# Performance work log

Hardware: AMD Instinct MI355X
Metric: run time of the kernel (lower is better)

The kernel has to match this reference:

```python
import jax, jax.numpy as jnp
import numpy as np

N = 50000
E = 600000


def gcn_conv(x, W, b, src, dst, n):
    # PyG GCNConv: h = x @ W; add self-loops; symmetric normalization; aggregate; + bias
    h = x @ W  # [N, out]
    deg = jnp.zeros((n,), h.dtype).at[dst].add(1.0) + 1.0  # self-loop included
    dinv = jax.lax.rsqrt(deg)  # deg >= 1, always finite
    coef = dinv[src] * dinv[dst]  # [E]
    msg = h[src] * coef[:, None]  # [E, out]  (the memory-bound gather)
    agg = jax.ops.segment_sum(msg, dst, num_segments=n)
    agg = agg + h * (dinv * dinv)[:, None]  # self-loop contribution
    return agg + b


def setup_inputs() -> dict:
    key = jax.random.key(0)
    ks = jax.random.split(key, 8)
    x = jax.random.normal(ks[0], (N, 128), dtype=jnp.float32)
    edge_index = jax.random.randint(ks[1], (2, E), 0, N, dtype=jnp.int64 if jax.config.jax_enable_x64 else jnp.int32)
    def glorot(k, fan_in, fan_out):
        s = jnp.sqrt(6.0 / (fan_in + fan_out))
        return jax.random.uniform(k, (fan_in, fan_out), jnp.float32, -s, s)
    W1 = glorot(ks[2], 128, 128)
    b1 = jnp.zeros((128,), jnp.float32)
    W2 = glorot(ks[3], 128, 64)
    b2 = jnp.zeros((64,), jnp.float32)
    W3 = glorot(ks[4], 64, 16)
    b3 = jnp.zeros((16,), jnp.float32)
    return {"x": x, "edge_index": edge_index, "W1": W1, "b1": b1, "W2": W2, "b2": b2, "W3": W3, "b3": b3}


def reference(x, edge_index, W1, b1, W2, b2, W3, b3):
    src, dst = edge_index[0], edge_index[1]
    n = x.shape[0]
    h = jax.nn.relu(gcn_conv(x, W1, b1, src, dst, n))
    h = jax.nn.relu(gcn_conv(h, W2, b2, src, dst, n))
    h = gcn_conv(h, W3, b3, src, dst, n)
    return h
```

## Files before the change

kernel.cpp:

```cpp
#include <hip/hip_runtime.h>
#include <hip/hip_fp16.h>
#include <type_traits>


typedef _Float16 f16x8 __attribute__((ext_vector_type(8)));
typedef float f32x4 __attribute__((ext_vector_type(4)));

#define CSR_CAP 32

__device__ inline float2 h2f(unsigned int u) {
  __half2 h = __builtin_bit_cast(__half2, u);
  return __half22float2(h);
}

__device__ inline void fma8h(float4& a0, float4& a1, const uint4& g, float w) {
  float2 f0 = h2f(g.x), f1 = h2f(g.y), f2 = h2f(g.z), f3 = h2f(g.w);
  a0.x = fmaf(f0.x, w, a0.x);
  a0.y = fmaf(f0.y, w, a0.y);
  a0.z = fmaf(f1.x, w, a0.z);
  a0.w = fmaf(f1.y, w, a0.w);
  a1.x = fmaf(f2.x, w, a1.x);
  a1.y = fmaf(f2.y, w, a1.y);
  a1.z = fmaf(f3.x, w, a1.z);
  a1.w = fmaf(f3.y, w, a1.w);
}

__device__ inline unsigned int pack2h(float x, float y) {
  __half2 h = __floats2half2_rn(x, y);
  return __builtin_bit_cast(unsigned int, h);
}

__device__ inline uint2 pack4h(const float4& v) {
  uint2 r;
  r.x = pack2h(v.x, v.y);
  r.y = pack2h(v.z, v.w);
  return r;
}

template <int K, int F, typename TIN>
__global__ __launch_bounds__(512) void gemm_mfma(const TIN* __restrict__ A,
                                                 const float* __restrict__ W,
                                                 __half* __restrict__ C16, int n,
                                                 int nwaves,
                                                 const int* __restrict__ src,
                                                 const int* __restrict__ dst,
                                                 int* __restrict__ cur,
                                                 unsigned short* __restrict__ csr,
                                                 int E) {
  constexpr int KP = K + 8;
  constexpr int KS = K / 32;
  constexpr int NT = F / 16;

  __shared__ __half Ws[F * KP];

  int t = threadIdx.x;

  if (t >= 256) {
    __syncthreads();
    int base = blockIdx.x * 256 + (t - 256);
    int stride = gridDim.x * 256;
    for (int e0 = base; e0 < E; e0 += 4 * stride) {
      int d[4], s[4];
      bool v[4];
#pragma unroll
      for (int u = 0; u < 4; ++u) {
        int e = e0 + u * stride;
        v[u] = e < E;
        int ee = v[u] ? e : 0;
        d[u] = dst[ee];
        s[u] = src[ee];
      }
      int pos[4];
#pragma unroll
      for (int u = 0; u < 4; ++u)
        if (v[u]) pos[u] = atomicAdd(&cur[d[u]], 1);
#pragma unroll
      for (int u = 0; u < 4; ++u)
        if (v[u]) {
          int p = pos[u] >= CSR_CAP ? CSR_CAP - 1 : pos[u];
          csr[(size_t)d[u] * CSR_CAP + p] = (unsigned short)s[u];
        }
    }
    return;
  }

  for (int i = t; i < K * F; i += 256) {
    int kk = i / F, nn = i % F;
    Ws[nn * KP + kk] = __float2half(W[i]);
  }
  __syncthreads();

  int wave = blockIdx.x * 4 + (t >> 6);
  if (wave >= nwaves) return;
  int lane = t & 63;
  int m = lane & 15;
  int quad = lane >> 4;

  int arow = wave * 16 + m;
  if (arow >= n) arow = n - 1;

  f16x8 af[KS];
  if constexpr (std::is_same_v<TIN, float>) {
#pragma unroll
    for (int ks = 0; ks < KS; ++ks) {
      const float* p = A + (size_t)arow * K + ks * 32 + quad * 8;
      float4 lo = *(const float4*)p;
      float4 hi = *(const float4*)(p + 4);
      f16x8 a;
      a[0] = (_Float16)lo.x; a[1] = (_Float16)lo.y;
      a[2] = (_Float16)lo.z; a[3] = (_Float16)lo.w;
      a[4] = (_Float16)hi.x; a[5] = (_Float16)hi.y;
      a[6] = (_Float16)hi.z; a[7] = (_Float16)hi.w;
      af[ks] = a;
    }
  } else {
#pragma unroll
    for (int ks = 0; ks < KS; ++ks)
      af[ks] = *(const f16x8*)(const void*)&A[(size_t)arow * K + ks * 32 + quad * 8];
  }

  f32x4 acc[NT];
#pragma unroll
  for (int nt = 0; nt < NT; ++nt) acc[nt] = (f32x4){0.f, 0.f, 0.f, 0.f};
#pragma unroll
  for (int nt = 0; nt < NT; ++nt)
#pragma unroll
    for (int ks = 0; ks < KS; ++ks) {
      f16x8 b = *(const f16x8*)(const void*)&Ws[(nt * 16 + m) * KP + ks * 32 + quad * 8];
      acc[nt] = __builtin_amdgcn_mfma_f32_16x16x32_f16(af[ks], b, acc[nt], 0, 0, 0);
    }

  int rbase = wave * 16 + quad * 4;
#pragma unroll
  for (int nt = 0; nt < NT; ++nt)
#pragma unroll
    for (int r = 0; r < 4; ++r) {
      int rr = rbase + r;
      if (rr < n) C16[(size_t)rr * F + nt * 16 + m] = __float2half(acc[nt][r]);
    }
}

template <int K, int F, int CPL, int EU>
__global__ __launch_bounds__(512) void aggmm(
    const __half* __restrict__ hprev, const float* __restrict__ W,
    const float* __restrict__ bias, const int* __restrict__ cnt,
    const unsigned short* __restrict__ csr, __half* __restrict__ C16, int n) {
  constexpr int KP = K + 8;
  constexpr int KS = K / 32;
  constexpr int NT = F / 16;
  constexpr int RS = K / 8;
  static_assert(8 * CPL == RS, "chunk coverage (8 chunk-lanes per half)");

  __shared__ __half Ws[F * KP];
  __shared__ __half As[32 * KP];

  int t = threadIdx.x;
  for (int i = t; i < K * F; i += 512) {
    int kk = i / F, nn = i % F;
    Ws[nn * KP + kk] = __float2half(W[i]);
  }

  int wid = t >> 6;
  int lane = t & 63;
  int nb = blockIdx.x * 32;

  {
    int ng = lane >> 4;
    int sl = lane & 15;
    int half = sl >> 3;
    int fl = sl & 7;
    int nib = wid * 4 + ng;
    int node = nb + nib;
    int nd = node < n ? node : n - 1;
    const uint4* h4 = (const uint4*)hprev;
    int c0 = cnt[nd];
    float di = rsqrtf((float)c0 + 1.0f);
    float sc = di * di;
    int cc = c0 < CSR_CAP ? c0 : CSR_CAP;
    float4 acc[CPL][2];
#pragma unroll
    for (int c = 0; c < CPL; ++c) {
      acc[c][0] = make_float4(0.f, 0.f, 0.f, 0.f);
      acc[c][1] = make_float4(0.f, 0.f, 0.f, 0.f);
    }
    if (half == 0) {
#pragma unroll
      for (int c = 0; c < CPL; ++c) {
        uint4 sv = h4[(size_t)nd * RS + fl + c * 8];
        fma8h(acc[c][0], acc[c][1], sv, sc);
      }
    }
    int j0 = nd * CSR_CAP;
    int e = j0 + cc;
    int j = j0 + half;
    int p[EU];
#pragma unroll
    for (int u = 0; u < EU; ++u) p[u] = csr[j + 2 * u];
    for (; j + 2 * EU - 2 < e;) {
      uint4 g[EU][CPL];
#pragma unroll
      for (int u = 0; u < EU; ++u)
#pragma unroll
        for (int c = 0; c < CPL; ++c) g[u][c] = h4[(size_t)p[u] * RS + fl + c * 8];
      int cs[EU];
#pragma unroll
      for (int u = 0; u < EU; ++u) cs[u] = cnt[p[u]];
      j += 2 * EU;
      int pn[EU];
#pragma unroll
      for (int u = 0; u < EU; ++u) pn[u] = csr[j + 2 * u];
#pragma unroll
      for (int u = 0; u < EU; ++u) {
        float w = rsqrtf((float)cs[u] + 1.0f) * di;
#pragma unroll
        for (int c = 0; c < CPL; ++c) fma8h(acc[c][0], acc[c][1], g[u][c], w);
      }
#pragma unroll
      for (int u = 0; u < EU; ++u) p[u] = pn[u];
    }
#pragma unroll
    for (int u = 0; u < EU; ++u) {
      if (j + 2 * u < e) {
        float w = rsqrtf((float)cnt[p[u]] + 1.0f) * di;
#pragma unroll
        for (int c = 0; c < CPL; ++c) {
          uint4 g = h4[(size_t)p[u] * RS + fl + c * 8];
          fma8h(acc[c][0], acc[c][1], g, w);
        }
      }
    }
#pragma unroll
    for (int c = 0; c < CPL; ++c) {
      acc[c][0].x += __shfl_xor(acc[c][0].x, 8);
      acc[c][0].y += __shfl_xor(acc[c][0].y, 8);
      acc[c][0].z += __shfl_xor(acc[c][0].z, 8);
      acc[c][0].w += __shfl_xor(acc[c][0].w, 8);
      acc[c][1].x += __shfl_xor(acc[c][1].x, 8);
      acc[c][1].y += __shfl_xor(acc[c][1].y, 8);
      acc[c][1].z += __shfl_xor(acc[c][1].z, 8);
      acc[c][1].w += __shfl_xor(acc[c][1].w, 8);
    }
    if (half == 0) {
#pragma unroll
      for (int c = 0; c < CPL; ++c) {
        int ch = fl + c * 8;
        float4 b0 = *(const float4*)&bias[ch * 8];
        float4 b1 = *(const float4*)&bias[ch * 8 + 4];
        float4 r0 = make_float4(fmaxf(acc[c][0].x + b0.x, 0.f), fmaxf(acc[c][0].y + b0.y, 0.f),
                                fmaxf(acc[c][0].z + b0.z, 0.f), fmaxf(acc[c][0].w + b0.w, 0.f));
        float4 r1 = make_float4(fmaxf(acc[c][1].x + b1.x, 0.f), fmaxf(acc[c][1].y + b1.y, 0.f),
                                fmaxf(acc[c][1].z + b1.z, 0.f), fmaxf(acc[c][1].w + b1.w, 0.f));
        uint2 lo = pack4h(r0), hi = pack4h(r1);
        uint4 pk;
        pk.x = lo.x; pk.y = lo.y; pk.z = hi.x; pk.w = hi.y;
        *(uint4*)&As[(size_t)nib * KP + ch * 8] = pk;
      }
    }
  }

  __syncthreads();

  if (wid < 2) {
    int m = lane & 15;
    int quad = lane >> 4;
    const __half* At = &As[(size_t)wid * 16 * KP];
    f16x8 af[KS];
#pragma unroll
    for (int ks = 0; ks < KS; ++ks)
      af[ks] = *(const f16x8*)(const void*)&At[m * KP + ks * 32 + quad * 8];

    f32x4 acc2[NT];
#pragma unroll
    for (int nt = 0; nt < NT; ++nt) acc2[nt] = (f32x4){0.f, 0.f, 0.f, 0.f};
#pragma unroll
    for (int nt = 0; nt < NT; ++nt)
#pragma unroll
      for (int ks = 0; ks < KS; ++ks) {
        f16x8 bfr = *(const f16x8*)(const void*)&Ws[(nt * 16 + m) * KP + ks * 32 + quad * 8];
        acc2[nt] = __builtin_amdgcn_mfma_f32_16x16x32_f16(af[ks], bfr, acc2[nt], 0, 0, 0);
      }

    int rbase = nb + wid * 16 + quad * 4;
#pragma unroll
    for (int nt = 0; nt < NT; ++nt)
#pragma unroll
      for (int r = 0; r < 4; ++r) {
        int rr = rbase + r;
        if (rr < n) C16[(size_t)rr * F + nt * 16 + m] = __float2half(acc2[nt][r]);
      }
  }
}

__global__ __launch_bounds__(256) void agg_final(
    const __half* __restrict__ h16, const int* __restrict__ cnt,
    const unsigned short* __restrict__ csr, const float* __restrict__ bias,
    float* __restrict__ out, int n) {
  int node = blockIdx.x * 64 + threadIdx.x / 4;
  int q = threadIdx.x & 3;
  int half = q >> 1;
  int fl = q & 1;
  bool valid = node < n;
  int nd = valid ? node : n - 1;

  const uint4* h4 = (const uint4*)h16;
  int c0 = cnt[nd];
  float di = rsqrtf((float)c0 + 1.0f);
  int cc = c0 < CSR_CAP ? c0 : CSR_CAP;
  float4 a0 = make_float4(0.f, 0.f, 0.f, 0.f);
  float4 a1 = make_float4(0.f, 0.f, 0.f, 0.f);
  if (half == 0) {
    uint4 sv = h4[(size_t)nd * 2 + fl];
    fma8h(a0, a1, sv, di * di);
  }
  int s = nd * CSR_CAP;
  int e = s + cc;
  int j = s + half;
  for (; j + 2 < e; j += 4) {
    int p0 = csr[j];
    int p1 = csr[j + 2];
    int ca = cnt[p0];
    int cb = cnt[p1];
    uint4 g0 = h4[(size_t)p0 * 2 + fl];
    uint4 g1 = h4[(size_t)p1 * 2 + fl];
    fma8h(a0, a1, g0, rsqrtf((float)ca + 1.0f) * di);
    fma8h(a0, a1, g1, rsqrtf((float)cb + 1.0f) * di);
  }
  for (; j < e; j += 2) {
    int p = csr[j];
    uint4 g = h4[(size_t)p * 2 + fl];
    fma8h(a0, a1, g, rsqrtf((float)cnt[p] + 1.0f) * di);
  }

  a0.x += __shfl_xor(a0.x, 2);
  a0.y += __shfl_xor(a0.y, 2);
  a0.z += __shfl_xor(a0.z, 2);
  a0.w += __shfl_xor(a0.w, 2);
  a1.x += __shfl_xor(a1.x, 2);
  a1.y += __shfl_xor(a1.y, 2);
  a1.z += __shfl_xor(a1.z, 2);
  a1.w += __shfl_xor(a1.w, 2);

  if (valid && half == 0) {
    float4 b0 = *(const float4*)&bias[fl * 8];
    float4 b1 = *(const float4*)&bias[fl * 8 + 4];
    float4 r0 = make_float4(a0.x + b0.x, a0.y + b0.y, a0.z + b0.z, a0.w + b0.w);
    float4 r1 = make_float4(a1.x + b1.x, a1.y + b1.y, a1.z + b1.z, a1.w + b1.w);
    float* op = &out[(size_t)node * 16 + fl * 8];
    *(float4*)op = r0;
    *(float4*)(op + 4) = r1;
  }
}


extern "C" void kernel_launch(void* const* d_in, const int* in_sizes, int n_in,
                              void* d_out, int out_size, void* d_ws, size_t ws_size,
                              hipStream_t stream) {
  const float* x = (const float*)d_in[0];
  const int* edge = (const int*)d_in[1];
  const float* W1 = (const float*)d_in[2];
  const float* b1 = (const float*)d_in[3];
  const float* W2 = (const float*)d_in[4];
  const float* b2 = (const float*)d_in[5];
  const float* W3 = (const float*)d_in[6];
  const float* b3 = (const float*)d_in[7];

  const int N = in_sizes[0] / 128;
  const int E = in_sizes[1] / 2;
  const int* src = edge;
  const int* dstp = edge + E;
  float* out = (float*)d_out;

  size_t off = 0;
  auto take = [&](size_t bytes) -> void* {
    void* r = (char*)d_ws + off;
    off += (bytes + 255) & ~(size_t)255;
    return r;
  };
  int* cur = (int*)take((size_t)N * 4);
  unsigned short* csr =
      (unsigned short*)take((size_t)N * CSR_CAP * 2 + 256);
  __half* t1 = (__half*)take((size_t)N * 128 * 2);
  __half* t2 = (__half*)take((size_t)N * 64 * 2);
  __half* t3 = (__half*)take((size_t)N * 16 * 2);

  hipMemsetAsync(d_ws, 0, ((size_t)N * 4 + 255) & ~(size_t)255, stream);

  int nwaves = (N + 15) / 16;
  int gblk = (nwaves + 3) / 4;
  int ablk = (N + 31) / 32;
  int fblk = (N + 63) / 64;

  gemm_mfma<128, 128, float><<<gblk, 512, 0, stream>>>(x, W1, t1, N, nwaves,
                                                       src, dstp, cur, csr, E);

  aggmm<128, 64, 2, 4><<<ablk, 512, 0, stream>>>(t1, W2, b1, cur, csr, t2, N);
  aggmm<64, 16, 1, 4><<<ablk, 512, 0, stream>>>(t2, W3, b2, cur, csr, t3, N);
  agg_final<<<fblk, 256, 0, stream>>>(t3, cur, csr, b3, out, N);
}
```

Measured before the change: 172.6 us.

## Prescale GEMM outputs by source dinv to drop per-edge degree lookups

Folds the source-side normalization dinv[src] into the producing GEMM epilogue, so the stored features are already scaled per row. Downstream aggregations then do plain sums over neighbors and multiply by dinv[dst] once at the end. This removes the per-edge cnt gather and rsqrt in the layer-3 aggregation and the final kernel. Layer 2 still uses per-edge weights because its input t1 from the first GEMM is not prescaled. The fp16 storage of prescaled values changes rounding slightly.

Result: no change. 175.7 us (+1.8%).

```diff
diff --git a/kernel.cpp b/kernel.cpp
--- a/kernel.cpp
+++ b/kernel.cpp
@@ -23,6 +23,12 @@
   a1.y = fmaf(f2.y, w, a1.y);
   a1.z = fmaf(f3.x, w, a1.z);
   a1.w = fmaf(f3.y, w, a1.w);
+}
+
+__device__ inline void add8h(float4& a0, float4& a1, const uint4& g) {
+  float2 f0 = h2f(g.x), f1 = h2f(g.y), f2 = h2f(g.z), f3 = h2f(g.w);
+  a0.x += f0.x; a0.y += f0.y; a0.z += f1.x; a0.w += f1.y;
+  a1.x += f2.x; a1.y += f2.y; a1.z += f3.x; a1.w += f3.y;
 }
 
 __device__ inline unsigned int pack2h(float x, float y) {
@@ -140,7 +146,7 @@
     }
 }
 
-template <int K, int F, int CPL, int EU>
+template <int K, int F, int CPL, int EU, bool PRE, bool SCOUT>
 __global__ __launch_bounds__(512) void aggmm(
     const __half* __restrict__ hprev, const float* __restrict__ W,
     const float* __restrict__ bias, const int* __restrict__ cnt,
@@ -175,7 +181,6 @@
     const uint4* h4 = (const uint4*)hprev;
     int c0 = cnt[nd];
     float di = rsqrtf((float)c0 + 1.0f);
-    float sc = di * di;
     int cc = c0 < CSR_CAP ? c0 : CSR_CAP;
     float4 acc[CPL][2];
 #pragma unroll
@@ -187,7 +192,10 @@
 #pragma unroll
       for (int c = 0; c < CPL; ++c) {
         uint4 sv = h4[(size_t)nd * RS + fl + c * 8];
-        fma8h(acc[c][0], acc[c][1], sv, sc);
+        if constexpr (PRE)
+          add8h(acc[c][0], acc[c][1], sv);
+        else
+          fma8h(acc[c][0], acc[c][1], sv, di * di);
       }
     }
     int j0 = nd * CSR_CAP;
@@ -203,17 +211,24 @@
 #pragma unroll
         for (int c = 0; c < CPL; ++c) g[u][c] = h4[(size_t)p[u] * RS + fl + c * 8];
       int cs[EU];
-#pragma unroll
-      for (int u = 0; u < EU; ++u) cs[u] = cnt[p[u]];
+      if constexpr (!PRE) {
+#pragma unroll
+        for (int u = 0; u < EU; ++u) cs[u] = cnt[p[u]];
+      }
       j += 2 * EU;
       int pn[EU];
 #pragma unroll
       for (int u = 0; u < EU; ++u) pn[u] = csr[j + 2 * u];
 #pragma unroll
       for (int u = 0; u < EU; ++u) {
-        float w = rsqrtf((float)cs[u] + 1.0f) * di;
-#pragma unroll
-        for (int c = 0; c < CPL; ++c) fma8h(acc[c][0], acc[c][1], g[u][c], w);
+        if constexpr (PRE) {
+#pragma unroll
+          for (int c = 0; c < CPL; ++c) add8h(acc[c][0], acc[c][1], g[u][c]);
+        } else {
+          float w = rsqrtf((float)cs[u] + 1.0f) * di;
+#pragma unroll
+          for (int c = 0; c < CPL; ++c) fma8h(acc[c][0], acc[c][1], g[u][c], w);
+        }
       }
 #pragma unroll
       for (int u = 0; u < EU; ++u) p[u] = pn[u];
@@ -221,11 +236,19 @@
 #pragma unroll
     for (int u = 0; u < EU; ++u) {
       if (j + 2 * u < e) {
-        float w = rsqrtf((float)cnt[p[u]] + 1.0f) * di;
-#pragma unroll
-        for (int c = 0; c < CPL; ++c) {
-          uint4 g = h4[(size_t)p[u] * RS + fl + c * 8];
-          fma8h(acc[c][0], acc[c][1], g, w);
+        if constexpr (PRE) {
+#pragma unroll
+          for (int c = 0; c < CPL; ++c) {
+            uint4 g = h4[(size_t)p[u] * RS + fl + c * 8];
+            add8h(acc[c][0], acc[c][1], g);
+          }
+        } else {
+          float w = rsqrtf((float)cnt[p[u]] + 1.0f) * di;
+#pragma unroll
+          for (int c = 0; c < CPL; ++c) {
+            uint4 g = h4[(size_t)p[u] * RS + fl + c * 8];
+            fma8h(acc[c][0], acc[c][1], g, w);
+          }
         }
       }
     }
@@ -241,15 +264,20 @@
       acc[c][1].w += __shfl_xor(acc[c][1].w, 8);
     }
     if (half == 0) {
+      float sc = PRE ? di : 1.0f;
 #pragma unroll
       for (int c = 0; c < CPL; ++c) {
         int ch = fl + c * 8;
         float4 b0 = *(const float4*)&bias[ch * 8];
         float4 b1 = *(const float4*)&bias[ch * 8 + 4];
-        float4 r0 = make_float4(fmaxf(acc[c][0].x + b0.x, 0.f), fmaxf(acc[c][0].y + b0.y, 0.f),
-                                fmaxf(acc[c][0].z + b0.z, 0.f), fmaxf(acc[c][0].w + b0.w, 0.f));
-        float4 r1 = make_float4(fmaxf(acc[c][1].x + b1.x, 0.f), fmaxf(acc[c][1].y + b1.y, 0.f),
-                                fmaxf(acc[c][1].z + b1.z, 0.f), fmaxf(acc[c][1].w + b1.w, 0.f));
+        float4 r0 = make_float4(fmaxf(acc[c][0].x * sc + b0.x, 0.f),
+                                fmaxf(acc[c][0].y * sc + b0.y, 0.f),
+                                fmaxf(acc[c][0].z * sc + b0.z, 0.f),
+                                fmaxf(acc[c][0].w * sc + b0.w, 0.f));
+        float4 r1 = make_float4(fmaxf(acc[c][1].x * sc + b1.x, 0.f),
+                                fmaxf(acc[c][1].y * sc + b1.y, 0.f),
+                                fmaxf(acc[c][1].z * sc + b1.z, 0.f),
+                                fmaxf(acc[c][1].w * sc + b1.w, 0.f));
         uint2 lo = pack4h(r0), hi = pack4h(r1);
         uint4 pk;
         pk.x = lo.x; pk.y = lo.y; pk.z = hi.x; pk.w = hi.y;
@@ -281,12 +309,23 @@
       }
 
     int rbase = nb + wid * 16 + quad * 4;
+    float rw[4];
+#pragma unroll
+    for (int r = 0; r < 4; ++r) {
+      if constexpr (SCOUT) {
+        int rr = rbase + r;
+        int rc = rr < n ? rr : n - 1;
+        rw[r] = rsqrtf((float)cnt[rc] + 1.0f);
+      } else {
+        rw[r] = 1.0f;
+      }
+    }
 #pragma unroll
     for (int nt = 0; nt < NT; ++nt)
 #pragma unroll
       for (int r = 0; r < 4; ++r) {
         int rr = rbase + r;
-        if (rr < n) C16[(size_t)rr * F + nt * 16 + m] = __float2half(acc2[nt][r]);
+        if (rr < n) C16[(size_t)rr * F + nt * 16 + m] = __float2half(acc2[nt][r] * rw[r]);
       }
   }
 }
@@ -310,7 +349,7 @@
   float4 a1 = make_float4(0.f, 0.f, 0.f, 0.f);
   if (half == 0) {
     uint4 sv = h4[(size_t)nd * 2 + fl];
-    fma8h(a0, a1, sv, di * di);
+    add8h(a0, a1, sv);
   }
   int s = nd * CSR_CAP;
   int e = s + cc;
@@ -318,17 +357,15 @@
   for (; j + 2 < e; j += 4) {
     int p0 = csr[j];
     int p1 = csr[j + 2];
-    int ca = cnt[p0];
-    int cb = cnt[p1];
     uint4 g0 = h4[(size_t)p0 * 2 + fl];
     uint4 g1 = h4[(size_t)p1 * 2 + fl];
-    fma8h(a0, a1, g0, rsqrtf((float)ca + 1.0f) * di);
-    fma8h(a0, a1, g1, rsqrtf((float)cb + 1.0f) * di);
+    add8h(a0, a1, g0);
+    add8h(a0, a1, g1);
   }
   for (; j < e; j += 2) {
     int p = csr[j];
     uint4 g = h4[(size_t)p * 2 + fl];
-    fma8h(a0, a1, g, rsqrtf((float)cnt[p] + 1.0f) * di);
+    add8h(a0, a1, g);
   }
 
   a0.x += __shfl_xor(a0.x, 2);
@@ -343,8 +380,10 @@
   if (valid && half == 0) {
     float4 b0 = *(const float4*)&bias[fl * 8];
     float4 b1 = *(const float4*)&bias[fl * 8 + 4];
-    float4 r0 = make_float4(a0.x + b0.x, a0.y + b0.y, a0.z + b0.z, a0.w + b0.w);
-    float4 r1 = make_float4(a1.x + b1.x, a1.y + b1.y, a1.z + b1.z, a1.w + b1.w);
+    float4 r0 = make_float4(a0.x * di + b0.x, a0.y * di + b0.y,
+                            a0.z * di + b0.z, a0.w * di + b0.w);
+    float4 r1 = make_float4(a1.x * di + b1.x, a1.y * di + b1.y,
+                            a1.z * di + b1.z, a1.w * di + b1.w);
     float* op = &out[(size_t)node * 16 + fl * 8];
     *(float4*)op = r0;
     *(float4*)(op + 4) = r1;
@@ -393,7 +432,7 @@
   gemm_mfma<128, 128, float><<<gblk, 512, 0, stream>>>(x, W1, t1, N, nwaves,
                                                        src, dstp, cur, csr, E);
 
-  aggmm<128, 64, 2, 4><<<ablk, 512, 0, stream>>>(t1, W2, b1, cur, csr, t2, N);
-  aggmm<64, 16, 1, 4><<<ablk, 512, 0, stream>>>(t2, W3, b2, cur, csr, t3, N);
+  aggmm<128, 64, 2, 4, false, true><<<ablk, 512, 0, stream>>>(t1, W2, b1, cur, csr, t2, N);
+  aggmm<64, 16, 1, 4, true, true><<<ablk, 512, 0, stream>>>(t2, W3, b2, cur, csr, t3, N);
   agg_final<<<fblk, 256, 0, stream>>>(t3, cur, csr, b3, out, N);
 }
```
